# Kernel optimization log

Hardware: AMD Instinct MI355X
Metric: run time of the kernel (lower is better)

The kernel has to match this reference:

```python
import jax, jax.numpy as jnp
import numpy as np

EPS = np.float32(np.finfo(float).eps)  # 2.220446049250313e-16, matches torch code
TOP_K = 2


def setup_inputs() -> dict:
    key = jax.random.key(0)
    ks = jax.random.split(key, 7)
    B, D, H, E = 8192, 1024, 4096, 8
    # init scales mirror the torch MLP init (std = sqrt(2/(m+n)), sqrt(1/m))
    return {
        "inp": jax.random.normal(ks[0], (B, D), dtype=jnp.float32),
        "gate_w": jax.random.normal(ks[1], (E, D), dtype=jnp.float32) * np.sqrt(1.0 / D).astype(np.float32),
        "gate_b": jax.random.normal(ks[2], (E,), dtype=jnp.float32) * 0.01,
        "W1": jax.random.normal(ks[3], (E, H, D), dtype=jnp.float32) * np.sqrt(2.0 / (H + D)).astype(np.float32),
        "b1": jax.random.normal(ks[4], (E, H), dtype=jnp.float32) * np.sqrt(1.0 / H).astype(np.float32),
        "W2": jax.random.normal(ks[5], (E, D, H), dtype=jnp.float32) * np.sqrt(2.0 / (D + H)).astype(np.float32),
        "b2": jax.random.normal(ks[6], (E, D), dtype=jnp.float32) * np.sqrt(1.0 / D).astype(np.float32),
    }


def _moe_forward(inp, gate_w, gate_b, W1, b1, W2, b2):
    B = inp.shape[0]
    E = gate_w.shape[0]
    # --- NaiveGate: linear -> top-k -> softmax -> scatter into dense gates ---
    logits = inp @ gate_w.T + gate_b                      # [B, E]
    top_vals, top_idx = jax.lax.top_k(logits, TOP_K)      # [B, k]
    top_gates = jax.nn.softmax(top_vals, axis=-1)         # top_k > 1 branch
    gates = jnp.zeros((B, E), dtype=jnp.float32)
    gates = gates.at[jnp.arange(B)[:, None], top_idx].set(top_gates)

    # --- Experts: 2-layer MLP, ReLU after every linear (sigmoid_layer=-1) ---
    h = jax.nn.relu(jnp.einsum('bd,ehd->ebh', inp, W1) + b1[:, None, :])   # [E, B, H]
    out = jax.nn.relu(jnp.einsum('ebh,edh->ebd', h, W2) + b2[:, None, :])  # [E, B, D]

    # --- SparseDispatcher.combine: exp -> gate-weighted scatter-sum -> +eps -> log ---
    # Dense-equivalent: gates are exactly zero for non-routed (token, expert)
    # pairs, so the weighted sum matches the sparse scatter exactly.
    combined = jnp.einsum('be,ebd->bd', gates, jnp.exp(out))
    return jnp.log(combined + EPS)


def reference(inp, gate_w, gate_b, W1, b1, W2, b2):
    return _moe_forward(inp, gate_w, gate_b, W1, b1, W2, b2)
```

## Files before the change

### kernel.cpp

```cpp
#include <hip/hip_runtime.h>
#include <hip/hip_bf16.h>
#include <math.h>

#define B_TOK 8192
#define DDIM  1024
#define HDIM  4096
#define NEXP  8
#define CAP   17408

typedef unsigned short u16;
using f32x4  = __attribute__((ext_vector_type(4))) float;
using bf16x8 = __attribute__((ext_vector_type(8))) short;

__device__ __forceinline__ u16 f2bf(float f) {
  union { float f; unsigned u; } v; v.f = f;
  unsigned r = v.u + 0x7FFFu + ((v.u >> 16) & 1u);
  return (u16)(r >> 16);
}

__device__ __forceinline__ void load_lds16(const void* g, void* l) {
  __builtin_amdgcn_global_load_lds((const __attribute__((address_space(1))) void*)g,
                                   (__attribute__((address_space(3))) void*)l,
                                   16, 0, 0);
}

__global__ __launch_bounds__(256) void cvt_kernel(const float4* __restrict__ src,
                                                  ushort4* __restrict__ dst, int n4) {
  for (int i = blockIdx.x * 256 + threadIdx.x; i < n4; i += gridDim.x * 256) {
    float4 v = src[i];
    ushort4 o;
    o.x = f2bf(v.x); o.y = f2bf(v.y); o.z = f2bf(v.z); o.w = f2bf(v.w);
    dst[i] = o;
  }
}

__global__ __launch_bounds__(256) void gate_kernel(
    const float* __restrict__ inp, const float* __restrict__ gw,
    const float* __restrict__ gb, int* __restrict__ tok_e,
    float* __restrict__ tok_g, int* __restrict__ counts)
{
  int gtid = blockIdx.x * 256 + threadIdx.x;
  int tok  = gtid >> 6;
  int lane = threadIdx.x & 63;
  if (tok >= B_TOK) return;
  const float4* X = (const float4*)(inp + (size_t)tok * DDIM);
  float4 x[4];
#pragma unroll
  for (int j = 0; j < 4; ++j) x[j] = X[j * 64 + lane];
  float lg[NEXP];
#pragma unroll
  for (int e = 0; e < NEXP; ++e) {
    const float4* W = (const float4*)(gw + e * DDIM);
    double s = 0.0;
#pragma unroll
    for (int j = 0; j < 4; ++j) {
      float4 w = W[j * 64 + lane];
      s += (double)x[j].x * w.x + (double)x[j].y * w.y
         + (double)x[j].z * w.z + (double)x[j].w * w.w;
    }
#pragma unroll
    for (int o = 32; o > 0; o >>= 1) s += __shfl_xor(s, o);
    lg[e] = (float)(s + (double)gb[e]);
  }
  if (lane == 0) {
    int i0 = 0; float v0 = lg[0];
#pragma unroll
    for (int e = 1; e < NEXP; ++e) if (lg[e] > v0) { v0 = lg[e]; i0 = e; }
    int i1 = -1; float v1 = -3.4e38f;
#pragma unroll
    for (int e = 0; e < NEXP; ++e) if (e != i0 && lg[e] > v1) { v1 = lg[e]; i1 = e; }
    float t   = __expf(v1 - v0);
    float inv = 1.0f / (1.0f + t);
    tok_e[2 * tok] = i0; tok_e[2 * tok + 1] = i1;
    tok_g[2 * tok] = inv; tok_g[2 * tok + 1] = t * inv;
    atomicAdd(&counts[i0], 1);
    atomicAdd(&counts[i1], 1);
  }
}

__global__ void scan_kernel(const int* __restrict__ counts, int* __restrict__ offs,
                            int* __restrict__ padded)
{
  if (threadIdx.x == 0 && blockIdx.x == 0) {
    int off = 0;
    for (int e = 0; e < NEXP; ++e) {
      offs[e] = off;
      int p = (counts[e] + 127) & ~127;
      padded[e] = p;
      off += p;
    }
  }
}

__global__ __launch_bounds__(256) void scatter_kernel(
    const int* __restrict__ tok_e, const float* __restrict__ tok_g,
    const int* __restrict__ offs, int* __restrict__ cursors,
    int* __restrict__ slot_token, float* __restrict__ slot_gate)
{
  int b = blockIdx.x * 256 + threadIdx.x;
  if (b >= B_TOK) return;
#pragma unroll
  for (int k = 0; k < 2; ++k) {
    int e   = tok_e[2 * b + k];
    float g = tok_g[2 * b + k];
    int pos = atomicAdd(&cursors[e], 1);
    int s   = offs[e] + pos;
    slot_token[s] = b;
    slot_gate[s]  = g;
  }
}


#define STAGE(bf_, kt_) do {                                              \
    _Pragma("unroll") for (int g = 0; g < 4; ++g) {                       \
      load_lds16(pAg[g] + (kt_) * 64, &As[bf_][g * 2048 + sdst]);          \
      load_lds16(pBg[g] + (kt_) * 64, &Bs[bf_][g * 2048 + sdst]);          \
    } } while (0)

#define VMW(n_) asm volatile("s_waitcnt vmcnt(" #n_ ")" ::: "memory")
#define SBAR __builtin_amdgcn_s_barrier()
#define SCHED0 __builtin_amdgcn_sched_barrier(0)

#define GEMM_BODY(NT_) do {                                               \
                                                 \
  STAGE(0, 0); STAGE(1, 1);                                               \
  VMW(8); SBAR; SCHED0;                                                   \
  _Pragma("unroll 1")                                                     \
  for (int t = 0; t < (NT_); ++t) {                                       \
    const int cur = t & 1;                                                \
    bf16x8 af[4][2], bfr[4][2];                                           \
    _Pragma("unroll") for (int m = 0; m < 4; ++m)                         \
      _Pragma("unroll") for (int kk = 0; kk < 2; ++kk)                    \
        af[m][kk] = *(const bf16x8*)&As[cur][(wm + m*16 + fr)*64          \
                                      + (((kk*4 + fq) ^ fr7) * 8)];       \
    _Pragma("unroll") for (int n = 0; n < 4; ++n)                         \
      _Pragma("unroll") for (int kk = 0; kk < 2; ++kk)                    \
        bfr[n][kk] = *(const bf16x8*)&Bs[cur][(wn + n*16 + fr)*64         \
                                      + (((kk*4 + fq) ^ fr7) * 8)];       \
    asm volatile("s_waitcnt lgkmcnt(0)" ::: "memory");                    \
    SCHED0;                                                               \
    SBAR; SCHED0;                    \
    if (t + 2 < (NT_)) STAGE(cur, t + 2);                                 \
    __builtin_amdgcn_s_setprio(1);                                        \
    _Pragma("unroll") for (int kk = 0; kk < 2; ++kk)                      \
    _Pragma("unroll") for (int m = 0; m < 4; ++m)                         \
    _Pragma("unroll") for (int n = 0; n < 4; ++n)                         \
      acc[m][n] = __builtin_amdgcn_mfma_f32_16x16x32_bf16(                \
          af[m][kk], bfr[n][kk], acc[m][n], 0, 0, 0);                     \
    __builtin_amdgcn_s_setprio(0);                                        \
    if (t + 2 < (NT_))      { VMW(8); }              \
    else if (t + 1 < (NT_)) { VMW(0); }                                   \
    SBAR; SCHED0;                                                         \
  } } while (0)

__global__ __launch_bounds__(256, 2) void gemm1_kernel(
    const u16* __restrict__ Xb, const u16* __restrict__ W1b,
    const float* __restrict__ b1, const int* __restrict__ slot_token,
    const int* __restrict__ offs, const int* __restrict__ padded,
    u16* __restrict__ Hb)
{
  const int h   = blockIdx.x + 32 * (blockIdx.y + 64 * blockIdx.z);
  const int e   = h & 7;
  const int r   = h >> 3;
  const int mi  = r >> 5;
  const int nti = r & 31;
  if (mi * 128 >= padded[e]) return;
  const int base_slot = offs[e] + mi * 128;
  const int n0 = nti * 128;
  const int NT = DDIM / 64;

  __shared__ __align__(16) u16 As[2][8192];
  __shared__ __align__(16) u16 Bs[2][8192];
  __shared__ int toks[128];

  const int tid = threadIdx.x;
  if (tid < 128) toks[tid] = slot_token[base_slot + tid];
  __syncthreads();

  const int srow = tid >> 3;
  const int scol = ((tid & 7) ^ (srow & 7)) * 8;
  const int sdst = tid * 8;
  const u16* pAg[4];
  const u16* pBg[4];
#pragma unroll
  for (int g = 0; g < 4; ++g) {
    int rr = g * 32 + srow;
    pAg[g] = Xb + (size_t)toks[rr] * DDIM + scol;
    pBg[g] = W1b + ((size_t)e * HDIM + (size_t)(n0 + rr)) * DDIM + scol;
  }

  const int wave = tid >> 6, lane = tid & 63;
  const int wm = (wave >> 1) * 64, wn = (wave & 1) * 64;
  const int fr = lane & 15, fq = lane >> 4, fr7 = fr & 7;

  f32x4 acc[4][4];
#pragma unroll
  for (int m = 0; m < 4; ++m)
#pragma unroll
    for (int n = 0; n < 4; ++n) acc[m][n] = f32x4{0.f, 0.f, 0.f, 0.f};

  GEMM_BODY(NT);

#pragma unroll
  for (int n = 0; n < 4; ++n) {
    int col = n0 + wn + n * 16 + fr;
    float bias = b1[e * HDIM + col];
#pragma unroll
    for (int m = 0; m < 4; ++m) {
      int row0 = wm + m * 16 + fq * 4;
#pragma unroll
      for (int j = 0; j < 4; ++j) {
        float v = acc[m][n][j] + bias;
        v = v > 0.f ? v : 0.f;
        Hb[(size_t)(base_slot + row0 + j) * HDIM + col] = f2bf(v);
      }
    }
  }
}

__global__ __launch_bounds__(256, 2) void gemm2_kernel(
    const u16* __restrict__ Hb, const u16* __restrict__ W2b,
    const float* __restrict__ b2, const float* __restrict__ slot_gate,
    const int* __restrict__ slot_token, const int* __restrict__ offs,
    const int* __restrict__ padded, float* __restrict__ out)
{
  const int h   = blockIdx.x + 8 * (blockIdx.y + 64 * blockIdx.z);
  const int e   = h & 7;
  const int r   = h >> 3;
  const int mi  = r >> 3;
  const int nti = r & 7;
  if (mi * 128 >= padded[e]) return;
  const int base_slot = offs[e] + mi * 128;
  const int n0 = nti * 128;
  const int NT = HDIM / 64;

  __shared__ __align__(16) u16 As[2][8192];
  __shared__ __align__(16) u16 Bs[2][8192];
  __shared__ int   toks[128];
  __shared__ float gts[128];

  const int tid = threadIdx.x;
  if (tid < 128) {
    toks[tid] = slot_token[base_slot + tid];
    gts[tid]  = slot_gate[base_slot + tid];
  }
  __syncthreads();

  const int srow = tid >> 3;
  const int scol = ((tid & 7) ^ (srow & 7)) * 8;
  const int sdst = tid * 8;
  const u16* pAg[4];
  const u16* pBg[4];
#pragma unroll
  for (int g = 0; g < 4; ++g) {
    int rr = g * 32 + srow;
    pAg[g] = Hb + (size_t)(base_slot + rr) * HDIM + scol;
    pBg[g] = W2b + ((size_t)e * DDIM + (size_t)(n0 + rr)) * HDIM + scol;
  }

  const int wave = tid >> 6, lane = tid & 63;
  const int wm = (wave >> 1) * 64, wn = (wave & 1) * 64;
  const int fr = lane & 15, fq = lane >> 4, fr7 = fr & 7;

  f32x4 acc[4][4];
#pragma unroll
  for (int m = 0; m < 4; ++m)
#pragma unroll
    for (int n = 0; n < 4; ++n) acc[m][n] = f32x4{0.f, 0.f, 0.f, 0.f};

  GEMM_BODY(NT);

#pragma unroll
  for (int n = 0; n < 4; ++n) {
    int col = n0 + wn + n * 16 + fr;
    float bias = b2[e * DDIM + col];
#pragma unroll
    for (int m = 0; m < 4; ++m) {
      int row0 = wm + m * 16 + fq * 4;
#pragma unroll
      for (int j = 0; j < 4; ++j) {
        int row = row0 + j;
        float v = acc[m][n][j] + bias;
        v = v > 0.f ? v : 0.f;
        float p = gts[row] * __expf(v);
        atomicAdd(&out[(size_t)toks[row] * DDIM + col], p);
      }
    }
  }
}

__global__ __launch_bounds__(256) void log_kernel(float4* __restrict__ out, int n4) {
  const float EPS = 2.220446049250313e-16f;
  for (int i = blockIdx.x * 256 + threadIdx.x; i < n4; i += gridDim.x * 256) {
    float4 v = out[i];
    v.x = logf(v.x + EPS);
    v.y = logf(v.y + EPS);
    v.z = logf(v.z + EPS);
    v.w = logf(v.w + EPS);
    out[i] = v;
  }
}

extern "C" void kernel_launch(void* const* d_in, const int* in_sizes, int n_in,
                              void* d_out, int out_size, void* d_ws, size_t ws_size,
                              hipStream_t stream)
{
  const float* inp = (const float*)d_in[0];
  const float* gw  = (const float*)d_in[1];
  const float* gb  = (const float*)d_in[2];
  const float* W1  = (const float*)d_in[3];
  const float* b1  = (const float*)d_in[4];
  const float* W2  = (const float*)d_in[5];
  const float* b2  = (const float*)d_in[6];
  float* out = (float*)d_out;

  char* ws = (char*)d_ws;
  size_t off = 0;
  auto alloc = [&](size_t bytes) {
    void* p = ws + off;
    off = (off + bytes + 255) & ~(size_t)255;
    return p;
  };
  u16*   Xb  = (u16*)alloc((size_t)B_TOK * DDIM * 2);
  u16*   W1b = (u16*)alloc((size_t)NEXP * HDIM * DDIM * 2);
  u16*   W2b = (u16*)alloc((size_t)NEXP * DDIM * HDIM * 2);
  u16*   Hb  = (u16*)alloc((size_t)CAP * HDIM * 2);
  int*   slot_token = (int*)alloc(CAP * 4);
  float* slot_gate  = (float*)alloc(CAP * 4);
  int*   tok_e = (int*)alloc(B_TOK * 2 * 4);
  float* tok_g = (float*)alloc(B_TOK * 2 * 4);
  int*   counts  = (int*)alloc(32);
  int*   offs    = (int*)alloc(32);
  int*   padded  = (int*)alloc(32);
  int*   cursors = (int*)alloc(32);

  (void)hipMemsetAsync(counts, 0, 32, stream);
  (void)hipMemsetAsync(cursors, 0, 32, stream);
  (void)hipMemsetAsync(slot_token, 0, CAP * 4, stream);
  (void)hipMemsetAsync(slot_gate, 0, CAP * 4, stream);
  (void)hipMemsetAsync(out, 0, (size_t)out_size * 4, stream);

  cvt_kernel<<<2048, 256, 0, stream>>>((const float4*)inp, (ushort4*)Xb, B_TOK * DDIM / 4);
  cvt_kernel<<<2048, 256, 0, stream>>>((const float4*)W1, (ushort4*)W1b, NEXP * HDIM * DDIM / 4);
  cvt_kernel<<<2048, 256, 0, stream>>>((const float4*)W2, (ushort4*)W2b, NEXP * DDIM * HDIM / 4);

  gate_kernel<<<B_TOK / 4, 256, 0, stream>>>(inp, gw, gb, tok_e, tok_g, counts);
  scan_kernel<<<1, 64, 0, stream>>>(counts, offs, padded);
  scatter_kernel<<<B_TOK / 256, 256, 0, stream>>>(tok_e, tok_g, offs, cursors,
                                                  slot_token, slot_gate);

  gemm1_kernel<<<dim3(32, 64, NEXP), 256, 0, stream>>>(
      Xb, W1b, b1, slot_token, offs, padded, Hb);
  gemm2_kernel<<<dim3(8, 64, NEXP), 256, 0, stream>>>(
      Hb, W2b, b2, slot_gate, slot_token, offs, padded, out);

  log_kernel<<<2048, 256, 0, stream>>>((float4*)out, out_size / 4);
}
```

Measured before the change: 840.8 us.

## Double-buffer MFMA register fragments to overlap LDS reads with compute

Result: slower. 886.2 us (+5.4%).

```diff
diff --git a/kernel.cpp b/kernel.cpp
--- a/kernel.cpp
+++ b/kernel.cpp
@@ -118,40 +118,55 @@
     } } while (0)
 
 #define VMW(n_) asm volatile("s_waitcnt vmcnt(" #n_ ")" ::: "memory")
-#define SBAR __builtin_amdgcn_s_barrier()
-#define SCHED0 __builtin_amdgcn_sched_barrier(0)
+#define SBAR do { __builtin_amdgcn_s_barrier();                           \
+                  __builtin_amdgcn_sched_barrier(0); } while (0)
+#define LGKM0 do { asm volatile("s_waitcnt lgkmcnt(0)" ::: "memory");     \
+                   __builtin_amdgcn_sched_barrier(0); } while (0)
+#define P1 __builtin_amdgcn_s_setprio(1)
+#define P0 __builtin_amdgcn_s_setprio(0)
+
+#define DSREAD(dst_, bf_) do {                                            \
+  _Pragma("unroll") for (int m = 0; m < 4; ++m)                           \
+    _Pragma("unroll") for (int kk = 0; kk < 2; ++kk)                      \
+      dst_##a[m][kk] = *(const bf16x8*)&As[bf_][(wm + m*16 + fr)*64       \
+                                        + (((kk*4 + fq) ^ fr7) * 8)];     \
+  _Pragma("unroll") for (int n = 0; n < 4; ++n)                           \
+    _Pragma("unroll") for (int kk = 0; kk < 2; ++kk)                      \
+      dst_##b[n][kk] = *(const bf16x8*)&Bs[bf_][(wn + n*16 + fr)*64       \
+                                        + (((kk*4 + fq) ^ fr7) * 8)];     \
+  } while (0)
+
+#define MFMA_SET(src_) do { P1;                                           \
+  _Pragma("unroll") for (int kk = 0; kk < 2; ++kk)                        \
+  _Pragma("unroll") for (int m = 0; m < 4; ++m)                           \
+  _Pragma("unroll") for (int n = 0; n < 4; ++n)                           \
+    acc[m][n] = __builtin_amdgcn_mfma_f32_16x16x32_bf16(                  \
+        src_##a[m][kk], src_##b[n][kk], acc[m][n], 0, 0, 0);              \
+  P0; } while (0)
+
+#define HALF(t_, cbuf_, nbuf_, CUR_, NXT_) do {                           \
+    if ((t_) + 2 < NT) { STAGE(cbuf_, (t_) + 2); VMW(8); }                \
+    else               { VMW(0); }                                        \
+    SBAR;                                                                 \
+    if ((t_) + 1 < NT) DSREAD(NXT_, nbuf_);                               \
+    MFMA_SET(CUR_);                                                       \
+    LGKM0;                                                                \
+    SBAR;                                                                 \
+  } while (0)
 
 #define GEMM_BODY(NT_) do {                                               \
-                                                 \
-  STAGE(0, 0); STAGE(1, 1);                                               \
-  VMW(8); SBAR; SCHED0;                                                   \
-  _Pragma("unroll 1")                                                     \
-  for (int t = 0; t < (NT_); ++t) {                                       \
-    const int cur = t & 1;                                                \
-    bf16x8 af[4][2], bfr[4][2];                                           \
-    _Pragma("unroll") for (int m = 0; m < 4; ++m)                         \
-      _Pragma("unroll") for (int kk = 0; kk < 2; ++kk)                    \
-        af[m][kk] = *(const bf16x8*)&As[cur][(wm + m*16 + fr)*64          \
-                                      + (((kk*4 + fq) ^ fr7) * 8)];       \
-    _Pragma("unroll") for (int n = 0; n < 4; ++n)                         \
-      _Pragma("unroll") for (int kk = 0; kk < 2; ++kk)                    \
-        bfr[n][kk] = *(const bf16x8*)&Bs[cur][(wn + n*16 + fr)*64         \
-                                      + (((kk*4 + fq) ^ fr7) * 8)];       \
-    asm volatile("s_waitcnt lgkmcnt(0)" ::: "memory");                    \
-    SCHED0;                                                               \
-    SBAR; SCHED0;                    \
-    if (t + 2 < (NT_)) STAGE(cur, t + 2);                                 \
-    __builtin_amdgcn_s_setprio(1);                                        \
-    _Pragma("unroll") for (int kk = 0; kk < 2; ++kk)                      \
-    _Pragma("unroll") for (int m = 0; m < 4; ++m)                         \
-    _Pragma("unroll") for (int n = 0; n < 4; ++n)                         \
-      acc[m][n] = __builtin_amdgcn_mfma_f32_16x16x32_bf16(                \
-          af[m][kk], bfr[n][kk], acc[m][n], 0, 0, 0);                     \
-    __builtin_amdgcn_s_setprio(0);                                        \
-    if (t + 2 < (NT_))      { VMW(8); }              \
-    else if (t + 1 < (NT_)) { VMW(0); }                                   \
-    SBAR; SCHED0;                                                         \
-  } } while (0)
+    const int NT = (NT_);                                                 \
+    STAGE(0, 0); STAGE(1, 1);                                             \
+    VMW(8); SBAR;                                                         \
+    DSREAD(fx, 0);                                                        \
+    LGKM0;                                                                \
+    SBAR;                                                                 \
+    _Pragma("unroll 1")                                                   \
+    for (int i = 0; i < NT / 2; ++i) {                                    \
+      const int t0 = 2 * i;                                               \
+      HALF(t0,     0, 1, fx, fy);                                         \
+      HALF(t0 + 1, 1, 0, fy, fx);                                         \
+    } } while (0)
 
 __global__ __launch_bounds__(256, 2) void gemm1_kernel(
     const u16* __restrict__ Xb, const u16* __restrict__ W1b,
@@ -167,7 +182,6 @@
   if (mi * 128 >= padded[e]) return;
   const int base_slot = offs[e] + mi * 128;
   const int n0 = nti * 128;
-  const int NT = DDIM / 64;
 
   __shared__ __align__(16) u16 As[2][8192];
   __shared__ __align__(16) u16 Bs[2][8192];
@@ -198,8 +212,9 @@
   for (int m = 0; m < 4; ++m)
 #pragma unroll
     for (int n = 0; n < 4; ++n) acc[m][n] = f32x4{0.f, 0.f, 0.f, 0.f};
-
-  GEMM_BODY(NT);
+  bf16x8 fxa[4][2], fxb[4][2], fya[4][2], fyb[4][2];
+
+  GEMM_BODY(DDIM / 64);
 
 #pragma unroll
   for (int n = 0; n < 4; ++n) {
@@ -232,7 +247,6 @@
   if (mi * 128 >= padded[e]) return;
   const int base_slot = offs[e] + mi * 128;
   const int n0 = nti * 128;
-  const int NT = HDIM / 64;
 
   __shared__ __align__(16) u16 As[2][8192];
   __shared__ __align__(16) u16 Bs[2][8192];
@@ -267,8 +281,9 @@
   for (int m = 0; m < 4; ++m)
 #pragma unroll
     for (int n = 0; n < 4; ++n) acc[m][n] = f32x4{0.f, 0.f, 0.f, 0.f};
-
-  GEMM_BODY(NT);
+  bf16x8 fxa[4][2], fxb[4][2], fya[4][2], fyb[4][2];
+
+  GEMM_BODY(HDIM / 64);
 
 #pragma unroll
   for (int n = 0; n < 4; ++n) {
```

## Load weight fragments directly to registers and triple-buffer activation tiles in LDS

Applied to the files above, without the earlier changes.

Result: slower. 1.042 ms (+23.9%).

```diff
diff --git a/kernel.cpp b/kernel.cpp
--- a/kernel.cpp
+++ b/kernel.cpp
@@ -112,46 +112,61 @@
 
 
 #define STAGE(bf_, kt_) do {                                              \
-    _Pragma("unroll") for (int g = 0; g < 4; ++g) {                       \
-      load_lds16(pAg[g] + (kt_) * 64, &As[bf_][g * 2048 + sdst]);          \
-      load_lds16(pBg[g] + (kt_) * 64, &Bs[bf_][g * 2048 + sdst]);          \
-    } } while (0)
-
-#define VMW(n_) asm volatile("s_waitcnt vmcnt(" #n_ ")" ::: "memory")
-#define SBAR __builtin_amdgcn_s_barrier()
-#define SCHED0 __builtin_amdgcn_sched_barrier(0)
-
-#define GEMM_BODY(NT_) do {                                               \
-                                                 \
-  STAGE(0, 0); STAGE(1, 1);                                               \
-  VMW(8); SBAR; SCHED0;                                                   \
-  _Pragma("unroll 1")                                                     \
-  for (int t = 0; t < (NT_); ++t) {                                       \
-    const int cur = t & 1;                                                \
-    bf16x8 af[4][2], bfr[4][2];                                           \
+    _Pragma("unroll") for (int g = 0; g < 4; ++g)                         \
+      load_lds16(pAg[g] + (kt_) * 64, &As[bf_][(g * 256 + tid) * 8]);      \
+  } while (0)
+
+#define LOADB(dst_, kt_) do {                                             \
+    _Pragma("unroll") for (int n = 0; n < 4; ++n)                         \
+      _Pragma("unroll") for (int kk = 0; kk < 2; ++kk)                    \
+        dst_[n][kk] = *(const bf16x8*)(pBl + (size_t)(n * 16) * KD        \
+                                       + (size_t)(kt_) * 64 + kk * 32);   \
+  } while (0)
+
+#define DSREAD_A(bf_) do {                                                \
     _Pragma("unroll") for (int m = 0; m < 4; ++m)                         \
       _Pragma("unroll") for (int kk = 0; kk < 2; ++kk)                    \
-        af[m][kk] = *(const bf16x8*)&As[cur][(wm + m*16 + fr)*64          \
+        af[m][kk] = *(const bf16x8*)&As[bf_][(wm + m*16 + fr)*64          \
                                       + (((kk*4 + fq) ^ fr7) * 8)];       \
-    _Pragma("unroll") for (int n = 0; n < 4; ++n)                         \
-      _Pragma("unroll") for (int kk = 0; kk < 2; ++kk)                    \
-        bfr[n][kk] = *(const bf16x8*)&Bs[cur][(wn + n*16 + fr)*64         \
-                                      + (((kk*4 + fq) ^ fr7) * 8)];       \
-    asm volatile("s_waitcnt lgkmcnt(0)" ::: "memory");                    \
-    SCHED0;                                                               \
-    SBAR; SCHED0;                    \
-    if (t + 2 < (NT_)) STAGE(cur, t + 2);                                 \
-    __builtin_amdgcn_s_setprio(1);                                        \
+  } while (0)
+
+#define MFMA_SET(B_) do { __builtin_amdgcn_s_setprio(1);                  \
     _Pragma("unroll") for (int kk = 0; kk < 2; ++kk)                      \
     _Pragma("unroll") for (int m = 0; m < 4; ++m)                         \
     _Pragma("unroll") for (int n = 0; n < 4; ++n)                         \
       acc[m][n] = __builtin_amdgcn_mfma_f32_16x16x32_bf16(                \
-          af[m][kk], bfr[n][kk], acc[m][n], 0, 0, 0);                     \
-    __builtin_amdgcn_s_setprio(0);                                        \
-    if (t + 2 < (NT_))      { VMW(8); }              \
-    else if (t + 1 < (NT_)) { VMW(0); }                                   \
-    SBAR; SCHED0;                                                         \
-  } } while (0)
+          af[m][kk], B_[n][kk], acc[m][n], 0, 0, 0);                      \
+    __builtin_amdgcn_s_setprio(0); } while (0)
+
+#define VMW(n_) asm volatile("s_waitcnt vmcnt(" #n_ ")" ::: "memory")
+#define SCHED0 __builtin_amdgcn_sched_barrier(0)
+#define SBAR do { SCHED0; __builtin_amdgcn_s_barrier(); SCHED0; } while (0)
+
+#define BODY(t_, BC_, BN_) do {                                           \
+    DSREAD_A(cb);                                                         \
+    if ((t_) + 2 < NT) STAGE(sb, (t_) + 2);                               \
+    if ((t_) + 1 < NT) LOADB(BN_, (t_) + 1);                              \
+    if ((t_) + 2 < NT)      { VMW(12); }                                  \
+    else if ((t_) + 1 < NT) { VMW(8); }                                   \
+    else                    { VMW(0); }                                   \
+    SCHED0;                                                               \
+    MFMA_SET(BC_);                                                        \
+    SBAR;                                                                 \
+    cb = (cb + 1 == 3) ? 0 : cb + 1;                                      \
+    sb = (sb + 1 == 3) ? 0 : sb + 1;                                      \
+  } while (0)
+
+#define GEMM_BODY(NT_) do {                                               \
+    const int NT = (NT_);                                                 \
+    STAGE(0, 0); STAGE(1, 1);                                             \
+    LOADB(bA, 0);                                                         \
+    VMW(12); SBAR;                                                        \
+    int cb = 0, sb = 2;                                                   \
+    _Pragma("unroll 1")                                                   \
+    for (int i = 0; i < NT / 2; ++i) {                                    \
+      BODY(2 * i,     bA, bB);                                            \
+      BODY(2 * i + 1, bB, bA);                                            \
+    } } while (0)
 
 __global__ __launch_bounds__(256, 2) void gemm1_kernel(
     const u16* __restrict__ Xb, const u16* __restrict__ W1b,
@@ -167,39 +182,35 @@
   if (mi * 128 >= padded[e]) return;
   const int base_slot = offs[e] + mi * 128;
   const int n0 = nti * 128;
-  const int NT = DDIM / 64;
-
-  __shared__ __align__(16) u16 As[2][8192];
-  __shared__ __align__(16) u16 Bs[2][8192];
+  const size_t KD = DDIM;
+
+  __shared__ __align__(16) u16 As[3][8192];
   __shared__ int toks[128];
 
   const int tid = threadIdx.x;
   if (tid < 128) toks[tid] = slot_token[base_slot + tid];
   __syncthreads();
 
-  const int srow = tid >> 3;
-  const int scol = ((tid & 7) ^ (srow & 7)) * 8;
-  const int sdst = tid * 8;
-  const u16* pAg[4];
-  const u16* pBg[4];
-#pragma unroll
-  for (int g = 0; g < 4; ++g) {
-    int rr = g * 32 + srow;
-    pAg[g] = Xb + (size_t)toks[rr] * DDIM + scol;
-    pBg[g] = W1b + ((size_t)e * HDIM + (size_t)(n0 + rr)) * DDIM + scol;
-  }
-
   const int wave = tid >> 6, lane = tid & 63;
   const int wm = (wave >> 1) * 64, wn = (wave & 1) * 64;
   const int fr = lane & 15, fq = lane >> 4, fr7 = fr & 7;
 
+  const u16* pAg[4];
+#pragma unroll
+  for (int g = 0; g < 4; ++g) {
+    int i = g * 256 + tid, rr = i >> 3, sl = i & 7;
+    pAg[g] = Xb + (size_t)toks[rr] * DDIM + (sl ^ (rr & 7)) * 8;
+  }
+  const u16* pBl = W1b + ((size_t)e * HDIM + (size_t)(n0 + wn + fr)) * DDIM + fq * 8;
+
   f32x4 acc[4][4];
 #pragma unroll
   for (int m = 0; m < 4; ++m)
 #pragma unroll
     for (int n = 0; n < 4; ++n) acc[m][n] = f32x4{0.f, 0.f, 0.f, 0.f};
-
-  GEMM_BODY(NT);
+  bf16x8 af[4][2], bA[4][2], bB[4][2];
+
+  GEMM_BODY(DDIM / 64);
 
 #pragma unroll
   for (int n = 0; n < 4; ++n) {
@@ -232,10 +243,9 @@
   if (mi * 128 >= padded[e]) return;
   const int base_slot = offs[e] + mi * 128;
   const int n0 = nti * 128;
-  const int NT = HDIM / 64;
-
-  __shared__ __align__(16) u16 As[2][8192];
-  __shared__ __align__(16) u16 Bs[2][8192];
+  const size_t KD = HDIM;
+
+  __shared__ __align__(16) u16 As[3][8192];
   __shared__ int   toks[128];
   __shared__ float gts[128];
 
@@ -246,29 +256,26 @@
   }
   __syncthreads();
 
-  const int srow = tid >> 3;
-  const int scol = ((tid & 7) ^ (srow & 7)) * 8;
-  const int sdst = tid * 8;
-  const u16* pAg[4];
-  const u16* pBg[4];
-#pragma unroll
-  for (int g = 0; g < 4; ++g) {
-    int rr = g * 32 + srow;
-    pAg[g] = Hb + (size_t)(base_slot + rr) * HDIM + scol;
-    pBg[g] = W2b + ((size_t)e * DDIM + (size_t)(n0 + rr)) * HDIM + scol;
-  }
-
   const int wave = tid >> 6, lane = tid & 63;
   const int wm = (wave >> 1) * 64, wn = (wave & 1) * 64;
   const int fr = lane & 15, fq = lane >> 4, fr7 = fr & 7;
 
+  const u16* pAg[4];
+#pragma unroll
+  for (int g = 0; g < 4; ++g) {
+    int i = g * 256 + tid, rr = i >> 3, sl = i & 7;
+    pAg[g] = Hb + (size_t)(base_slot + rr) * HDIM + (sl ^ (rr & 7)) * 8;
+  }
+  const u16* pBl = W2b + ((size_t)e * DDIM + (size_t)(n0 + wn + fr)) * HDIM + fq * 8;
+
   f32x4 acc[4][4];
 #pragma unroll
   for (int m = 0; m < 4; ++m)
 #pragma unroll
     for (int n = 0; n < 4; ++n) acc[m][n] = f32x4{0.f, 0.f, 0.f, 0.f};
-
-  GEMM_BODY(NT);
+  bf16x8 af[4][2], bA[4][2], bB[4][2];
+
+  GEMM_BODY(HDIM / 64);
 
 #pragma unroll
   for (int n = 0; n < 4; ++n) {
```
